# Performance work log

Measured on AMD Instinct MI355X. Metric: run time of the kernel, lower is better.

## Reference

```python
import jax, jax.numpy as jnp
import numpy as np

N_EMBD = 1024
N_HEAD = 16
HEAD_DIM = N_EMBD // N_HEAD
LN_EPS = 1e-5


def setup_inputs() -> dict:
    key = jax.random.key(0)
    ks = jax.random.split(key, 8)
    C = N_EMBD
    s = 0.02
    return {
        "x": jax.random.normal(ks[0], (2, 2048, C), dtype=jnp.float32),
        "ln1_g": jnp.ones((C,), jnp.float32),
        "ln1_b": jnp.zeros((C,), jnp.float32),
        "qkv_w": jax.random.normal(ks[1], (C, 3 * C), jnp.float32) * s,
        "qkv_b": jnp.zeros((3 * C,), jnp.float32),
        "out_w": jax.random.normal(ks[2], (C, C), jnp.float32) * s,
        "out_b": jnp.zeros((C,), jnp.float32),
        "ln2_g": jnp.ones((C,), jnp.float32),
        "ln2_b": jnp.zeros((C,), jnp.float32),
        "fc1_w": jax.random.normal(ks[3], (C, 4 * C), jnp.float32) * s,
        "fc1_b": jnp.zeros((4 * C,), jnp.float32),
        "fc2_w": jax.random.normal(ks[4], (4 * C, C), jnp.float32) * s,
        "fc2_b": jnp.zeros((C,), jnp.float32),
    }


def _layernorm(x, g, b):
    mu = jnp.mean(x, axis=-1, keepdims=True)
    var = jnp.var(x, axis=-1, keepdims=True)
    return (x - mu) * jax.lax.rsqrt(var + LN_EPS) * g + b


def reference(x, ln1_g, ln1_b, qkv_w, qkv_b, out_w, out_b,
              ln2_g, ln2_b, fc1_w, fc1_b, fc2_w, fc2_b):
    B, T, C = x.shape
    H, D = N_HEAD, HEAD_DIM

    # --- attention (pre-norm) ---
    h = _layernorm(x, ln1_g, ln1_b)
    qkv = h @ qkv_w + qkv_b                      # [B,T,3C]
    q, k, v = jnp.split(qkv, 3, axis=-1)
    q = q.reshape(B, T, H, D).transpose(0, 2, 1, 3)  # [B,H,T,D]
    k = k.reshape(B, T, H, D).transpose(0, 2, 1, 3)
    v = v.reshape(B, T, H, D).transpose(0, 2, 1, 3)

    attn = jnp.einsum('bhqd,bhkd->bhqk', q, k) / jnp.sqrt(jnp.float32(D))
    causal = jnp.tril(jnp.ones((T, T), bool))
    attn = jnp.where(causal, attn, -jnp.inf)
    attn = jax.nn.softmax(attn, axis=-1)
    o = jnp.einsum('bhqk,bhkd->bhqd', attn, v)   # [B,H,T,D]
    o = o.transpose(0, 2, 1, 3).reshape(B, T, C)
    x = x + (o @ out_w + out_b)

    # --- FFN (pre-norm) ---
    h = _layernorm(x, ln2_g, ln2_b)
    h = jax.nn.gelu(h @ fc1_w + fc1_b, approximate=False)
    x = x + (h @ fc2_w + fc2_b)
    return x
```

## Files before the change

### kernel.cpp

```cpp
#include <hip/hip_runtime.h>
#include <hip/hip_bf16.h>
#include <cstdint>

#define DEVI __device__ __forceinline__

typedef __attribute__((ext_vector_type(8))) short bf16x8;
typedef __attribute__((ext_vector_type(4))) float f32x4;

DEVI ushort f2bf(float f){
  union { float f; uint32_t u; } c; c.f = f;
  uint32_t u = c.u + 0x7fffu + ((c.u >> 16) & 1u);
  return (ushort)(u >> 16);
}

DEVI void gload_lds16(const void* g, void* l){
  __builtin_amdgcn_global_load_lds((const __attribute__((address_space(1))) void*)g,
                                   (__attribute__((address_space(3))) void*)l,
                                   16, 0, 0);
}

__global__ __launch_bounds__(256)
void transpose_cast(const float* __restrict__ in, ushort* __restrict__ out, int R, int C){
  __shared__ float tile[32][33];
  const int tx = threadIdx.x & 31, ty = threadIdx.x >> 5;
  const int bx = blockIdx.x * 32, by = blockIdx.y * 32;
  #pragma unroll
  for (int i = 0; i < 4; ++i)
    tile[ty + i*8][tx] = in[(size_t)(by + ty + i*8) * C + bx + tx];
  __syncthreads();
  #pragma unroll
  for (int i = 0; i < 4; ++i)
    out[(size_t)(bx + ty + i*8) * R + by + tx] = f2bf(tile[tx][ty + i*8]);
}

__global__ __launch_bounds__(256)
void ln_kernel(const float* __restrict__ x, const float* __restrict__ g,
               const float* __restrict__ b, ushort* __restrict__ out){
  const int row = blockIdx.x, tid = threadIdx.x;
  const float4 v = ((const float4*)(x + (size_t)row * 1024))[tid];
  float s  = v.x + v.y + v.z + v.w;
  float ss = v.x*v.x + v.y*v.y + v.z*v.z + v.w*v.w;
  #pragma unroll
  for (int off = 32; off > 0; off >>= 1){
    s  += __shfl_down(s,  off);
    ss += __shfl_down(ss, off);
  }
  __shared__ float red[8];
  const int wave = tid >> 6, lane = tid & 63;
  if (lane == 0){ red[wave] = s; red[4 + wave] = ss; }
  __syncthreads();
  s  = red[0] + red[1] + red[2] + red[3];
  ss = red[4] + red[5] + red[6] + red[7];
  const float mean = s * (1.0f/1024.0f);
  const float var  = ss * (1.0f/1024.0f) - mean*mean;
  const float rstd = rsqrtf(var + 1e-5f);
  const float4 gv = ((const float4*)g)[tid];
  const float4 bv = ((const float4*)b)[tid];
  ushort4 o;
  o.x = f2bf((v.x - mean) * rstd * gv.x + bv.x);
  o.y = f2bf((v.y - mean) * rstd * gv.y + bv.y);
  o.z = f2bf((v.z - mean) * rstd * gv.z + bv.z);
  o.w = f2bf((v.w - mean) * rstd * gv.w + bv.w);
  ((ushort4*)(out + (size_t)row * 1024))[tid] = o;
}

constexpr int BM = 128, BN = 128, BK = 32;
enum { EPI_QKV = 0, EPI_RES = 1, EPI_GELU = 2 };

template<int EPI>
__global__ __launch_bounds__(256, 2)
void gemm_bt(const ushort* __restrict__ A, const ushort* __restrict__ Bt,
             const float* __restrict__ bias, const float* __restrict__ resid,
             void* __restrict__ outp, int M, int N, int K)
{
  __shared__ ushort sA[BM*BK];
  __shared__ ushort sB[BN*BK];
  const int tid  = threadIdx.x;
  const int wave = tid >> 6, lane = tid & 63;
  const int l15 = lane & 15, g = lane >> 4;
  const int nbn = N / BN;
  const int mb = (blockIdx.x / nbn) * BM;
  const int nb = (blockIdx.x % nbn) * BN;
  const int wm = (wave >> 1) * 64, wn = (wave & 1) * 64;
  f32x4 acc[4][4] = {};
  const int arow = mb + (tid >> 2);
  const int brow = nb + (tid >> 2);
  const int kcol = (tid & 3) * 8;

  for (int kb = 0; kb < K; kb += BK){
    gload_lds16(A  + (size_t)arow      * K + kb + kcol, &sA[wave*512]);
    gload_lds16(A  + (size_t)(arow+64) * K + kb + kcol, &sA[2048 + wave*512]);
    gload_lds16(Bt + (size_t)brow      * K + kb + kcol, &sB[wave*512]);
    gload_lds16(Bt + (size_t)(brow+64) * K + kb + kcol, &sB[2048 + wave*512]);
    __syncthreads();
    bf16x8 af[4], bfv[4];
    const bf16x8* pA = (const bf16x8*)sA;
    const bf16x8* pB = (const bf16x8*)sB;
    #pragma unroll
    for (int i = 0; i < 4; ++i) af[i]  = pA[(wm + i*16 + l15)*4 + g];
    #pragma unroll
    for (int j = 0; j < 4; ++j) bfv[j] = pB[(wn + j*16 + l15)*4 + g];
    #pragma unroll
    for (int i = 0; i < 4; ++i)
      #pragma unroll
      for (int j = 0; j < 4; ++j)
        acc[i][j] = __builtin_amdgcn_mfma_f32_16x16x32_bf16(af[i], bfv[j], acc[i][j], 0, 0, 0);
    __syncthreads();
  }

  #pragma unroll
  for (int i = 0; i < 4; ++i){
    #pragma unroll
    for (int j = 0; j < 4; ++j){
      const int col = nb + wn + j*16 + l15;
      #pragma unroll
      for (int r = 0; r < 4; ++r){
        const int row = mb + wm + i*16 + g*4 + r;
        float vv = acc[i][j][r] + bias[col];
        if constexpr (EPI == EPI_RES){
          ((float*)outp)[(size_t)row * N + col] = vv + resid[(size_t)row * N + col];
        } else if constexpr (EPI == EPI_GELU){
          const float ge = 0.5f * vv * (1.0f + erff(vv * 0.70710678118f));
          ((ushort*)outp)[(size_t)row * N + col] = f2bf(ge);
        } else {
          const int which = col >> 10, c = col & 1023;
          const int head = c >> 6, d = c & 63;
          const int bb = row >> 11, t = row & 2047;
          ((ushort*)outp)[(size_t)which * 4194304 +
                          (((size_t)(bb*16 + head)) * 2048 + t) * 64 + d] = f2bf(vv);
        }
      }
    }
  }
}

__global__ __launch_bounds__(256, 2)
void attn_kernel(const ushort* __restrict__ Q, const ushort* __restrict__ K,
                 const ushort* __restrict__ V, ushort* __restrict__ O)
{
  constexpr int T = 2048, D = 64, LD = 72;
  __shared__ ushort sK[64*LD];
  __shared__ ushort sV[64*LD];
  __shared__ ushort sP[4][16*LD];
  const int tid = threadIdx.x, wave = tid >> 6, lane = tid & 63;
  const int l15 = lane & 15, g = lane >> 4;
  const int qt = blockIdx.x, bh = blockIdx.y;
  const size_t base = (size_t)bh * T * D;

  bf16x8 qf[2];
  {
    const bf16x8* Qv = (const bf16x8*)(Q + base + (size_t)(qt*64 + wave*16 + l15) * D);
    qf[0] = Qv[g];
    qf[1] = Qv[g + 4];
  }
  f32x4 oa[4] = {};
  float m_r[4], l_r[4];
  #pragma unroll
  for (int r = 0; r < 4; ++r){ m_r[r] = -1e30f; l_r[r] = 0.f; }

  for (int kt = 0; kt <= qt; ++kt){
    {
      const int key = tid >> 2, d0 = (tid & 3) * 16;
      const ushort* src = K + base + (size_t)(kt*64 + key) * D + d0;
      *(bf16x8*)&sK[key*LD + d0]     = *(const bf16x8*)src;
      *(bf16x8*)&sK[key*LD + d0 + 8] = *(const bf16x8*)(src + 8);
      const ushort* vs = V + base + (size_t)(kt*64 + key) * D + d0;
      ushort tmp[16];
      *(bf16x8*)&tmp[0] = *(const bf16x8*)vs;
      *(bf16x8*)&tmp[8] = *(const bf16x8*)(vs + 8);
      #pragma unroll
      for (int j = 0; j < 16; ++j) sV[(d0 + j)*LD + key] = tmp[j];
    }
    __syncthreads();

    f32x4 sf[4] = {};
    #pragma unroll
    for (int cf = 0; cf < 4; ++cf)
      #pragma unroll
      for (int kk = 0; kk < 2; ++kk){
        const bf16x8 kb = *(const bf16x8*)&sK[(cf*16 + l15)*LD + g*8 + kk*32];
        sf[cf] = __builtin_amdgcn_mfma_f32_16x16x32_bf16(qf[kk], kb, sf[cf], 0, 0, 0);
      }

    float p[4][4], rmax[4];
    const int qrow0 = qt*64 + wave*16 + g*4;
    const bool diag = (kt == qt);
    #pragma unroll
    for (int r = 0; r < 4; ++r) rmax[r] = -1e30f;
    #pragma unroll
    for (int cf = 0; cf < 4; ++cf)
      #pragma unroll
      for (int r = 0; r < 4; ++r){
        float s = sf[cf][r] * 0.125f;
        if (diag && (kt*64 + cf*16 + l15) > (qrow0 + r)) s = -1e30f;
        p[cf][r] = s;
        rmax[r] = fmaxf(rmax[r], s);
      }
    #pragma unroll
    for (int off = 1; off < 16; off <<= 1)
      #pragma unroll
      for (int r = 0; r < 4; ++r)
        rmax[r] = fmaxf(rmax[r], __shfl_xor(rmax[r], off));
    float alpha[4], lsum[4];
    #pragma unroll
    for (int r = 0; r < 4; ++r){
      const float mn = fmaxf(m_r[r], rmax[r]);
      alpha[r] = __expf(m_r[r] - mn);
      m_r[r] = mn;
      lsum[r] = 0.f;
    }
    #pragma unroll
    for (int cf = 0; cf < 4; ++cf)
      #pragma unroll
      for (int r = 0; r < 4; ++r){
        const float e = __expf(p[cf][r] - m_r[r]);
        p[cf][r] = e;
        lsum[r] += e;
      }
    #pragma unroll
    for (int off = 1; off < 16; off <<= 1)
      #pragma unroll
      for (int r = 0; r < 4; ++r)
        lsum[r] += __shfl_xor(lsum[r], off);
    #pragma unroll
    for (int r = 0; r < 4; ++r) l_r[r] = l_r[r]*alpha[r] + lsum[r];
    #pragma unroll
    for (int cf = 0; cf < 4; ++cf)
      #pragma unroll
      for (int r = 0; r < 4; ++r) oa[cf][r] *= alpha[r];

    #pragma unroll
    for (int cf = 0; cf < 4; ++cf)
      #pragma unroll
      for (int r = 0; r < 4; ++r)
        sP[wave][(g*4 + r)*LD + cf*16 + l15] = f2bf(p[cf][r]);
    __syncthreads();

    bf16x8 pa[2];
    pa[0] = *(const bf16x8*)&sP[wave][l15*LD + g*8];
    pa[1] = *(const bf16x8*)&sP[wave][l15*LD + g*8 + 32];
    #pragma unroll
    for (int cf = 0; cf < 4; ++cf)
      #pragma unroll
      for (int kk = 0; kk < 2; ++kk){
        const bf16x8 vb = *(const bf16x8*)&sV[(cf*16 + l15)*LD + g*8 + kk*32];
        oa[cf] = __builtin_amdgcn_mfma_f32_16x16x32_bf16(pa[kk], vb, oa[cf], 0, 0, 0);
      }
    __syncthreads();
  }

  const int bb = bh >> 4, h = bh & 15;
  #pragma unroll
  for (int cf = 0; cf < 4; ++cf)
    #pragma unroll
    for (int r = 0; r < 4; ++r){
      const int row = qt*64 + wave*16 + g*4 + r;
      O[((size_t)bb * T + row) * 1024 + h*64 + cf*16 + l15] = f2bf(oa[cf][r] / l_r[r]);
    }
}

extern "C" void kernel_launch(void* const* d_in, const int* in_sizes, int n_in,
                              void* d_out, int out_size, void* d_ws, size_t ws_size,
                              hipStream_t stream)
{
  const float* x     = (const float*)d_in[0];
  const float* ln1_g = (const float*)d_in[1];
  const float* ln1_b = (const float*)d_in[2];
  const float* qkv_w = (const float*)d_in[3];
  const float* qkv_b = (const float*)d_in[4];
  const float* out_w = (const float*)d_in[5];
  const float* out_b = (const float*)d_in[6];
  const float* ln2_g = (const float*)d_in[7];
  const float* ln2_b = (const float*)d_in[8];
  const float* fc1_w = (const float*)d_in[9];
  const float* fc1_b = (const float*)d_in[10];
  const float* fc2_w = (const float*)d_in[11];
  const float* fc2_b = (const float*)d_in[12];

  char* ws = (char*)d_ws;
  ushort* qkvwt = (ushort*)(ws + 0);
  ushort* outwt = (ushort*)(ws + 6291456);
  ushort* fc1wt = (ushort*)(ws + 8388608);
  ushort* fc2wt = (ushort*)(ws + 16777216);
  float*  x2    = (float*) (ws + 25165824);
  ushort* hbuf  = (ushort*)(ws + 41943040);
  ushort* qbuf  = (ushort*)(ws + 50331648);
  ushort* kbuf  = qbuf + 4194304;
  ushort* vbuf  = qbuf + 8388608;
  ushort* aout  = (ushort*)(ws + 75497472);
  ushort* h3    = (ushort*)(ws + 50331648);

  transpose_cast<<<dim3(96, 32),  256, 0, stream>>>(qkv_w, qkvwt, 1024, 3072);
  transpose_cast<<<dim3(32, 32),  256, 0, stream>>>(out_w, outwt, 1024, 1024);
  transpose_cast<<<dim3(128, 32), 256, 0, stream>>>(fc1_w, fc1wt, 1024, 4096);
  transpose_cast<<<dim3(32, 128), 256, 0, stream>>>(fc2_w, fc2wt, 4096, 1024);

  ln_kernel<<<4096, 256, 0, stream>>>(x, ln1_g, ln1_b, hbuf);
  gemm_bt<EPI_QKV><<<32*24, 256, 0, stream>>>(hbuf, qkvwt, qkv_b, nullptr, qbuf, 4096, 3072, 1024);
  attn_kernel<<<dim3(32, 32), 256, 0, stream>>>(qbuf, kbuf, vbuf, aout);
  gemm_bt<EPI_RES><<<32*8, 256, 0, stream>>>(aout, outwt, out_b, x, x2, 4096, 1024, 1024);
  ln_kernel<<<4096, 256, 0, stream>>>(x2, ln2_g, ln2_b, hbuf);
  gemm_bt<EPI_GELU><<<32*32, 256, 0, stream>>>(hbuf, fc1wt, fc1_b, nullptr, h3, 4096, 4096, 1024);
  gemm_bt<EPI_RES><<<32*8, 256, 0, stream>>>(h3, fc2wt, fc2_b, x2, (float*)d_out, 4096, 1024, 4096);
}
```

Measured before the change: 464.8 us.

## Pair causal query tiles per block and share K/V loads in attention

Each attention block now handles two query tiles, qt and 31-qt, so every block does the same amount of causal work and each K/V tile loaded into shared memory serves both query tiles. The V transpose store now writes packed 32-bit pairs instead of single 16-bit values. P is packed via a lane shuffle into 32-bit LDS writes, and the __syncthreads between the P store and the PV MFMA is removed, relying on sP being private to each wave. The grid is halved to 16x32 blocks, which lowers parallelism, and each block holds two sets of accumulators, which raises register pressure.

```diff
diff --git a/kernel.cpp b/kernel.cpp
--- a/kernel.cpp
+++ b/kernel.cpp
@@ -138,41 +138,33 @@
 void attn_kernel(const ushort* __restrict__ Q, const ushort* __restrict__ K,
                  const ushort* __restrict__ V, ushort* __restrict__ O)
 {
-  constexpr int T = 2048, D = 64, LD = 72;
+  constexpr int T = 2048, D = 64, LD = 72, NT = 32;
   __shared__ ushort sK[64*LD];
   __shared__ ushort sV[64*LD];
   __shared__ ushort sP[4][16*LD];
   const int tid = threadIdx.x, wave = tid >> 6, lane = tid & 63;
   const int l15 = lane & 15, g = lane >> 4;
-  const int qt = blockIdx.x, bh = blockIdx.y;
+  const int qtA = blockIdx.x;
+  const int qtB = NT - 1 - qtA;
+  const int bh = blockIdx.y;
   const size_t base = (size_t)bh * T * D;
 
-  bf16x8 qf[2];
+  bf16x8 qfA[2], qfB[2];
   {
-    const bf16x8* Qv = (const bf16x8*)(Q + base + (size_t)(qt*64 + wave*16 + l15) * D);
-    qf[0] = Qv[g];
-    qf[1] = Qv[g + 4];
-  }
-  f32x4 oa[4] = {};
-  float m_r[4], l_r[4];
-  #pragma unroll
-  for (int r = 0; r < 4; ++r){ m_r[r] = -1e30f; l_r[r] = 0.f; }
-
-  for (int kt = 0; kt <= qt; ++kt){
-    {
-      const int key = tid >> 2, d0 = (tid & 3) * 16;
-      const ushort* src = K + base + (size_t)(kt*64 + key) * D + d0;
-      *(bf16x8*)&sK[key*LD + d0]     = *(const bf16x8*)src;
-      *(bf16x8*)&sK[key*LD + d0 + 8] = *(const bf16x8*)(src + 8);
-      const ushort* vs = V + base + (size_t)(kt*64 + key) * D + d0;
-      ushort tmp[16];
-      *(bf16x8*)&tmp[0] = *(const bf16x8*)vs;
-      *(bf16x8*)&tmp[8] = *(const bf16x8*)(vs + 8);
-      #pragma unroll
-      for (int j = 0; j < 16; ++j) sV[(d0 + j)*LD + key] = tmp[j];
-    }
-    __syncthreads();
-
+    const bf16x8* QA = (const bf16x8*)(Q + base + (size_t)(qtA*64 + wave*16 + l15) * D);
+    qfA[0] = QA[g]; qfA[1] = QA[g + 4];
+    const bf16x8* QB = (const bf16x8*)(Q + base + (size_t)(qtB*64 + wave*16 + l15) * D);
+    qfB[0] = QB[g]; qfB[1] = QB[g + 4];
+  }
+  f32x4 oaA[4] = {}, oaB[4] = {};
+  float mA[4], lA[4], mB[4], lB[4];
+  #pragma unroll
+  for (int r = 0; r < 4; ++r){ mA[r] = mB[r] = -1e30f; lA[r] = lB[r] = 0.f; }
+
+  const int skey = tid >> 2, sd0 = (tid & 3) * 16;
+  const int kp = tid & 31,  dv0 = (tid >> 5) * 8;
+
+  auto tile_step = [&](int kt, int qt, const bf16x8* qf, f32x4* oa, float* m_r, float* l_r){
     f32x4 sf[4] = {};
     #pragma unroll
     for (int cf = 0; cf < 4; ++cf)
@@ -181,7 +173,6 @@
         const bf16x8 kb = *(const bf16x8*)&sK[(cf*16 + l15)*LD + g*8 + kk*32];
         sf[cf] = __builtin_amdgcn_mfma_f32_16x16x32_bf16(qf[kk], kb, sf[cf], 0, 0, 0);
       }
-
     float p[4][4], rmax[4];
     const int qrow0 = qt*64 + wave*16 + g*4;
     const bool diag = (kt == qt);
@@ -229,13 +220,22 @@
       #pragma unroll
       for (int r = 0; r < 4; ++r) oa[cf][r] *= alpha[r];
 
-    #pragma unroll
-    for (int cf = 0; cf < 4; ++cf)
-      #pragma unroll
-      for (int r = 0; r < 4; ++r)
-        sP[wave][(g*4 + r)*LD + cf*16 + l15] = f2bf(p[cf][r]);
-    __syncthreads();
-
+    uint32_t pk[16];
+    #pragma unroll
+    for (int cf = 0; cf < 4; ++cf)
+      #pragma unroll
+      for (int r = 0; r < 4; ++r){
+        const float e = p[cf][r];
+        const float o = __shfl_xor(e, 1);
+        pk[cf*4 + r] = (uint32_t)f2bf(e) | ((uint32_t)f2bf(o) << 16);
+      }
+    if (!(lane & 1)){
+      #pragma unroll
+      for (int cf = 0; cf < 4; ++cf)
+        #pragma unroll
+        for (int r = 0; r < 4; ++r)
+          *(uint32_t*)&sP[wave][(g*4 + r)*LD + cf*16 + l15] = pk[cf*4 + r];
+    }
     bf16x8 pa[2];
     pa[0] = *(const bf16x8*)&sP[wave][l15*LD + g*8];
     pa[1] = *(const bf16x8*)&sP[wave][l15*LD + g*8 + 32];
@@ -246,7 +246,24 @@
         const bf16x8 vb = *(const bf16x8*)&sV[(cf*16 + l15)*LD + g*8 + kk*32];
         oa[cf] = __builtin_amdgcn_mfma_f32_16x16x32_bf16(pa[kk], vb, oa[cf], 0, 0, 0);
       }
+  };
+
+  for (int kt = 0; kt <= qtB; ++kt){
+    const ushort* ks = K + base + (size_t)(kt*64 + skey) * D + sd0;
+    *(bf16x8*)&sK[skey*LD + sd0]     = *(const bf16x8*)ks;
+    *(bf16x8*)&sK[skey*LD + sd0 + 8] = *(const bf16x8*)(ks + 8);
+    const ushort* vs = V + base + (size_t)(kt*64 + 2*kp) * D + dv0;
+    const bf16x8 va = *(const bf16x8*)vs;
+    const bf16x8 vb = *(const bf16x8*)(vs + D);
+    #pragma unroll
+    for (int j = 0; j < 8; ++j){
+      const uint32_t pr = (uint32_t)(ushort)va[j] | ((uint32_t)(ushort)vb[j] << 16);
+      *(uint32_t*)&sV[(dv0 + j)*LD + 2*kp] = pr;
+    }
     __syncthreads();
+    tile_step(kt, qtB, qfB, oaB, mB, lB);
+    if (kt <= qtA) tile_step(kt, qtA, qfA, oaA, mA, lA);
+    __syncthreads();
   }
 
   const int bb = bh >> 4, h = bh & 15;
@@ -254,8 +271,10 @@
   for (int cf = 0; cf < 4; ++cf)
     #pragma unroll
     for (int r = 0; r < 4; ++r){
-      const int row = qt*64 + wave*16 + g*4 + r;
-      O[((size_t)bb * T + row) * 1024 + h*64 + cf*16 + l15] = f2bf(oa[cf][r] / l_r[r]);
+      const int rowB = qtB*64 + wave*16 + g*4 + r;
+      O[((size_t)bb * T + rowB) * 1024 + h*64 + cf*16 + l15] = f2bf(oaB[cf][r] / lB[r]);
+      const int rowA = qtA*64 + wave*16 + g*4 + r;
+      O[((size_t)bb * T + rowA) * 1024 + h*64 + cf*16 + l15] = f2bf(oaA[cf][r] / lA[r]);
     }
 }
 
@@ -297,7 +316,7 @@
 
   ln_kernel<<<4096, 256, 0, stream>>>(x, ln1_g, ln1_b, hbuf);
   gemm_bt<EPI_QKV><<<32*24, 256, 0, stream>>>(hbuf, qkvwt, qkv_b, nullptr, qbuf, 4096, 3072, 1024);
-  attn_kernel<<<dim3(32, 32), 256, 0, stream>>>(qbuf, kbuf, vbuf, aout);
+  attn_kernel<<<dim3(16, 32), 256, 0, stream>>>(qbuf, kbuf, vbuf, aout);
   gemm_bt<EPI_RES><<<32*8, 256, 0, stream>>>(aout, outwt, out_b, x, x2, 4096, 1024, 1024);
   ln_kernel<<<4096, 256, 0, stream>>>(x2, ln2_g, ln2_b, hbuf);
   gemm_bt<EPI_GELU><<<32*32, 256, 0, stream>>>(hbuf, fc1wt, fc1_b, nullptr, h3, 4096, 4096, 1024);
```

After: 424.7 us. 8.6% less time.
